# Optimization experiments

Hardware: AMD Instinct MI355X
Metric: run time of the kernel (lower is better)

## Reference

```python
import jax, jax.numpy as jnp
import numpy as np

B, H, W, C = 8, 32, 32, 512


def setup_inputs() -> dict:
    key = jax.random.key(0)
    ks = jax.random.split(key, 7)
    x = jax.random.normal(ks[0], (B, H, W, C), dtype=jnp.float32)
    conv_w = jax.random.normal(ks[1], (C, C), dtype=jnp.float32) * 0.02
    conv_b = jnp.zeros((C,), dtype=jnp.float32)
    q_w = jax.random.normal(ks[2], (C, C), dtype=jnp.float32) * 0.02
    q_b = jnp.zeros((C,), dtype=jnp.float32)
    k_w = jax.random.normal(ks[3], (C, C), dtype=jnp.float32) * 0.02
    k_b = jnp.zeros((C,), dtype=jnp.float32)
    return {"x": x, "conv_w": conv_w, "conv_b": conv_b,
            "q_w": q_w, "q_b": q_b, "k_w": k_w, "k_b": k_b}


def reference(x, conv_w, conv_b, q_w, q_b, k_w, k_b):
    # x: [B,H,W,C] channels-last (torch permutes to BCHW; we keep BHWC).
    b, h, w, c = x.shape
    hw = h * w
    scale = 1.0 / (c ** 0.5)
    # 1x1 conv + residual (weight layout: [out_ch, in_ch])
    xr = jnp.einsum('bhwc,oc->bhwo', x, conv_w) + conv_b + x
    # query / key 1x1 convs, flattened to (B*HW, C)
    q = (jnp.einsum('bhwc,oc->bhwo', xr, q_w) + q_b).reshape(b * hw, c)
    k = (jnp.einsum('bhwc,oc->bhwo', xr, k_w) + k_b).reshape(b * hw, c)
    # cross-batch affinity: (B*HW, B*HW)
    aff = (q @ k.T) * scale
    # per-(query-batch, pixel) block sums over key batches: (B, HW, B)
    s = aff.reshape(b, hw, b, hw).sum(-1)
    total = s.sum(-1)                                   # sum over all keys
    own = s[jnp.arange(b), :, jnp.arange(b)]            # own-batch block sum, (B, HW)
    rep = (total - own) / ((b - 1) * hw)                # masked mean excluding own block
    rmin = rep.min(axis=1, keepdims=True)
    rmax = rep.max(axis=1, keepdims=True)
    rep = (rep - rmin) / (rmax - rmin)                  # per-batch min-max norm
    thresh = 0.65
    return jax.nn.sigmoid((rep - thresh) / 0.15)        # (B, HW)
```

## Files before the change

### kernel.cpp

```cpp
#include <hip/hip_runtime.h>
#include <math.h>


#define BATCH 8
#define HW    1024
#define CH    512
#define SPLITS 64

__device__ __forceinline__ float dot4(float4 a, float4 b) {
    return a.x * b.x + a.y * b.y + a.z * b.z + a.w * b.w;
}

__global__ void k_xsum(const float* __restrict__ x, float* __restrict__ part) {
    int b = blockIdx.x >> 5, s = blockIdx.x & 31;
    int rg = threadIdx.x >> 7, col = threadIdx.x & 127;
    const float4* x4 = (const float4*)(x + ((size_t)(b * HW + s * 32 + rg * 8)) * CH);
    float4 acc; acc.x = acc.y = acc.z = acc.w = 0.f;
    #pragma unroll
    for (int r = 0; r < 8; ++r) {
        float4 v = x4[r * 128 + col];
        acc.x += v.x; acc.y += v.y; acc.z += v.z; acc.w += v.w;
    }
    __shared__ float4 sh[384];
    if (rg > 0) sh[(rg - 1) * 128 + col] = acc;
    __syncthreads();
    if (rg == 0) {
        #pragma unroll
        for (int j = 0; j < 3; ++j) {
            float4 o = sh[j * 128 + col];
            acc.x += o.x; acc.y += o.y; acc.z += o.z; acc.w += o.w;
        }
        ((float4*)part)[(size_t)(b * 32 + s) * 128 + col] = acc;
    }
}

__global__ void k_red(const float* __restrict__ part, float* __restrict__ xsum) {
    int b = blockIdx.x >> 2, chunk = blockIdx.x & 3;
    int c4 = threadIdx.x & 31, sg = threadIdx.x >> 5;
    const float4* p4 = (const float4*)part;
    float4 acc; acc.x = acc.y = acc.z = acc.w = 0.f;
    #pragma unroll
    for (int j = 0; j < 4; ++j) {
        int s = sg * 4 + j;
        float4 v = p4[(size_t)(b * 32 + s) * 128 + chunk * 32 + c4];
        acc.x += v.x; acc.y += v.y; acc.z += v.z; acc.w += v.w;
    }
    __shared__ float4 sh[8][32];
    sh[sg][c4] = acc;
    __syncthreads();
    if (threadIdx.x < 32) {
        float4 t = sh[0][c4];
        #pragma unroll
        for (int g = 1; g < 8; ++g) {
            float4 v = sh[g][c4];
            t.x += v.x; t.y += v.y; t.z += v.z; t.w += v.w;
        }
        ((float4*)xsum)[b * 128 + chunk * 32 + c4] = t;
    }
}

__global__ void k_t1(const float* __restrict__ xsum, const float* __restrict__ conv_w,
                     const float* __restrict__ conv_b, float* __restrict__ t1g) {
    int t = threadIdx.x;
    int b = blockIdx.x >> 7;
    int wv = t >> 6, lane = t & 63;
    __shared__ float ysh[CH];
    for (int c = t; c < CH; c += 256) {
        float tot = 0.f;
        #pragma unroll
        for (int bb = 0; bb < BATCH; ++bb) tot += xsum[bb * CH + c];
        ysh[c] = tot - xsum[b * CH + c];
    }
    __syncthreads();
    const float4* y4 = (const float4*)ysh;
    float4 ya = y4[lane], yb = y4[lane + 64];
    int o = (blockIdx.x & 127) * 4 + wv;
    const float4* w4 = (const float4*)(conv_w + (size_t)o * CH);
    float acc = dot4(ya, w4[lane]) + dot4(yb, w4[lane + 64]);
    #pragma unroll
    for (int off = 32; off; off >>= 1) acc += __shfl_xor(acc, off);
    if (lane == 0) t1g[b * CH + o] = acc + ysh[o] + 7168.f * conv_b[o];
}

__global__ void k_t2(const float* __restrict__ t1g, const float* __restrict__ k_w,
                     const float* __restrict__ k_b, float* __restrict__ t2g) {
    int t = threadIdx.x;
    int b = blockIdx.x >> 7;
    int wv = t >> 6, lane = t & 63;
    __shared__ float t1sh[CH];
    for (int c = t; c < CH; c += 256) t1sh[c] = t1g[b * CH + c];
    __syncthreads();
    const float4* a4 = (const float4*)t1sh;
    float4 aa = a4[lane], ab = a4[lane + 64];
    int o = (blockIdx.x & 127) * 4 + wv;
    const float4* w4 = (const float4*)(k_w + (size_t)o * CH);
    float acc = dot4(aa, w4[lane]) + dot4(ab, w4[lane + 64]);
    #pragma unroll
    for (int off = 32; off; off >>= 1) acc += __shfl_xor(acc, off);
    if (lane == 0) t2g[b * CH + o] = acc + 7168.f * k_b[o];
}

__global__ void k_wv(const float* __restrict__ t2g, const float* __restrict__ q_w,
                     float* __restrict__ wg) {
    int b = blockIdx.x >> 3, qc = blockIdx.x & 7;
    int t = threadIdx.x;
    __shared__ float t2sh[CH];
    __shared__ float ps[512];
    t2sh[t] = t2g[b * CH + t];
    __syncthreads();
    int c = qc * 64 + (t & 63), r0 = (t >> 6) * 64;
    float acc = 0.f;
    #pragma unroll 8
    for (int j = 0; j < 64; ++j) acc += q_w[(size_t)(r0 + j) * CH + c] * t2sh[r0 + j];
    ps[t] = acc;
    __syncthreads();
    if (t < 64) {
        float s = 0.f;
        #pragma unroll
        for (int k2 = 0; k2 < 8; ++k2) s += ps[k2 * 64 + t];
        wg[b * CH + qc * 64 + t] = s;
    }
}

__global__ void k_uv(const float* __restrict__ wg, const float* __restrict__ conv_w,
                     float* __restrict__ u) {
    int b = blockIdx.x >> 3, qc = blockIdx.x & 7;
    int t = threadIdx.x;
    __shared__ float wsh[CH];
    __shared__ float ps[512];
    wsh[t] = wg[b * CH + t];
    __syncthreads();
    int c = qc * 64 + (t & 63), r0 = (t >> 6) * 64;
    float acc = 0.f;
    #pragma unroll 8
    for (int j = 0; j < 64; ++j) acc += conv_w[(size_t)(r0 + j) * CH + c] * wsh[r0 + j];
    ps[t] = acc;
    __syncthreads();
    if (t < 64) {
        float s = 0.f;
        #pragma unroll
        for (int k2 = 0; k2 < 8; ++k2) s += ps[k2 * 64 + t];
        u[b * CH + qc * 64 + t] = s + wsh[qc * 64 + t];
    }
}

__global__ void k_dpass(const float* __restrict__ x, const float* __restrict__ u,
                        float* __restrict__ dvals, float* __restrict__ bmn,
                        float* __restrict__ bmx) {
    int s = blockIdx.x, b = blockIdx.y;
    int lane = threadIdx.x & 63, wv = threadIdx.x >> 6;
    const float4* u4 = (const float4*)(u + b * CH);
    float4 ua = u4[lane], ub = u4[lane + 64];
    __shared__ float sd[16];
    #pragma unroll
    for (int it = 0; it < 4; ++it) {
        int row = s * 16 + it * 4 + wv;
        const float4* x4 = (const float4*)(x + ((size_t)(b * HW + row)) * CH);
        float acc = dot4(x4[lane], ua) + dot4(x4[lane + 64], ub);
        #pragma unroll
        for (int off = 32; off; off >>= 1) acc += __shfl_xor(acc, off);
        if (lane == 0) {
            dvals[b * HW + row] = acc;
            sd[it * 4 + wv] = acc;
        }
    }
    __syncthreads();
    if (threadIdx.x == 0) {
        float mn = sd[0], mx = sd[0];
        #pragma unroll
        for (int i = 1; i < 16; ++i) {
            mn = fminf(mn, sd[i]); mx = fmaxf(mx, sd[i]);
        }
        bmn[b * SPLITS + s] = mn;
        bmx[b * SPLITS + s] = mx;
    }
}

__global__ void k_out(const float* __restrict__ dvals, const float* __restrict__ bmn,
                      const float* __restrict__ bmx, float* __restrict__ out) {
    int b = blockIdx.x, t = threadIdx.x;
    __shared__ float smn, smx;
    if (t < 64) {
        float mn = bmn[b * SPLITS + t];
        float mx = bmx[b * SPLITS + t];
        #pragma unroll
        for (int off = 32; off; off >>= 1) {
            mn = fminf(mn, __shfl_xor(mn, off));
            mx = fmaxf(mx, __shfl_xor(mx, off));
        }
        if (t == 0) { smn = mn; smx = mx; }
    }
    __syncthreads();
    float rmin = smn, inv = 1.f / (smx - smn);
    for (int i = t; i < HW; i += blockDim.x) {
        float d = dvals[b * HW + i];
        float rn = (d - rmin) * inv;
        float z = (rn - 0.65f) * (1.f / 0.15f);
        out[b * HW + i] = 1.f / (1.f + expf(-z));
    }
}

extern "C" void kernel_launch(void* const* d_in, const int* in_sizes, int n_in,
                              void* d_out, int out_size, void* d_ws, size_t ws_size,
                              hipStream_t stream) {
    const float* x      = (const float*)d_in[0];
    const float* conv_w = (const float*)d_in[1];
    const float* conv_b = (const float*)d_in[2];
    const float* q_w    = (const float*)d_in[3];
    const float* k_w    = (const float*)d_in[5];
    const float* k_b    = (const float*)d_in[6];
    float* out = (float*)d_out;

    float* ws    = (float*)d_ws;
    float* part  = ws;
    float* xsum  = part + 256 * CH;
    float* t1g   = xsum + BATCH * CH;
    float* t2g   = t1g + BATCH * CH;
    float* wg    = t2g + BATCH * CH;
    float* u     = wg  + BATCH * CH;
    float* dvals = u   + BATCH * CH;
    float* bmn   = dvals + BATCH * HW;
    float* bmx   = bmn + BATCH * SPLITS;

    hipLaunchKernelGGL(k_xsum,  dim3(256),           dim3(512), 0, stream, x, part);
    hipLaunchKernelGGL(k_red,   dim3(32),            dim3(256), 0, stream, part, xsum);
    hipLaunchKernelGGL(k_t1,    dim3(1024),          dim3(256), 0, stream, xsum, conv_w, conv_b, t1g);
    hipLaunchKernelGGL(k_t2,    dim3(1024),          dim3(256), 0, stream, t1g, k_w, k_b, t2g);
    hipLaunchKernelGGL(k_wv,    dim3(64),            dim3(512), 0, stream, t2g, q_w, wg);
    hipLaunchKernelGGL(k_uv,    dim3(64),            dim3(512), 0, stream, wg, conv_w, u);
    hipLaunchKernelGGL(k_dpass, dim3(SPLITS, BATCH), dim3(256), 0, stream, x, u, dvals, bmn, bmx);
    hipLaunchKernelGGL(k_out,   dim3(BATCH),         dim3(256), 0, stream, dvals, bmn, bmx, out);
}
```

Before: 98.59 us.

## Fuse two-stage column sum into one kernel and widen small kernels

The partial-sum kernel and its separate reduction kernel become one kernel: each block owns a 32-column chunk of one batch, sums all 1024 rows in registers, and reduces through shared memory. This removes a launch and the round trip through the partials workspace. It also vectorises the shared-memory staging in k_t1 and k_t2 with float4 and spreads k_out over 64 blocks instead of 8. The risk is that the fused column sum runs only 128 blocks with strided 128-byte row segments, which may lower achieved memory bandwidth on the 16 MB read.

```diff
diff --git a/kernel.cpp b/kernel.cpp
--- a/kernel.cpp
+++ b/kernel.cpp
@@ -11,51 +11,39 @@
     return a.x * b.x + a.y * b.y + a.z * b.z + a.w * b.w;
 }
 
-__global__ void k_xsum(const float* __restrict__ x, float* __restrict__ part) {
-    int b = blockIdx.x >> 5, s = blockIdx.x & 31;
-    int rg = threadIdx.x >> 7, col = threadIdx.x & 127;
-    const float4* x4 = (const float4*)(x + ((size_t)(b * HW + s * 32 + rg * 8)) * CH);
+__global__ void k_xsum(const float* __restrict__ x, float* __restrict__ xsum) {
+    int b = blockIdx.x >> 4, chunk = blockIdx.x & 15;
+    int t = threadIdx.x;
+    int col4 = t & 7, rg = t >> 3;
+    const float4* x4 = (const float4*)(x + (size_t)b * HW * CH) + chunk * 8 + col4;
     float4 acc; acc.x = acc.y = acc.z = acc.w = 0.f;
     #pragma unroll
-    for (int r = 0; r < 8; ++r) {
-        float4 v = x4[r * 128 + col];
+    for (int i = 0; i < 16; ++i) {
+        float4 v = x4[(size_t)(rg + (i << 6)) * 128];
         acc.x += v.x; acc.y += v.y; acc.z += v.z; acc.w += v.w;
     }
-    __shared__ float4 sh[384];
-    if (rg > 0) sh[(rg - 1) * 128 + col] = acc;
-    __syncthreads();
-    if (rg == 0) {
-        #pragma unroll
-        for (int j = 0; j < 3; ++j) {
-            float4 o = sh[j * 128 + col];
-            acc.x += o.x; acc.y += o.y; acc.z += o.z; acc.w += o.w;
-        }
-        ((float4*)part)[(size_t)(b * 32 + s) * 128 + col] = acc;
-    }
-}
-
-__global__ void k_red(const float* __restrict__ part, float* __restrict__ xsum) {
-    int b = blockIdx.x >> 2, chunk = blockIdx.x & 3;
-    int c4 = threadIdx.x & 31, sg = threadIdx.x >> 5;
-    const float4* p4 = (const float4*)part;
-    float4 acc; acc.x = acc.y = acc.z = acc.w = 0.f;
-    #pragma unroll
-    for (int j = 0; j < 4; ++j) {
-        int s = sg * 4 + j;
-        float4 v = p4[(size_t)(b * 32 + s) * 128 + chunk * 32 + c4];
-        acc.x += v.x; acc.y += v.y; acc.z += v.z; acc.w += v.w;
-    }
-    __shared__ float4 sh[8][32];
-    sh[sg][c4] = acc;
-    __syncthreads();
-    if (threadIdx.x < 32) {
-        float4 t = sh[0][c4];
-        #pragma unroll
-        for (int g = 1; g < 8; ++g) {
-            float4 v = sh[g][c4];
-            t.x += v.x; t.y += v.y; t.z += v.z; t.w += v.w;
-        }
-        ((float4*)xsum)[b * 128 + chunk * 32 + c4] = t;
+    __shared__ float4 sh[64][8];
+    sh[rg][col4] = acc;
+    __syncthreads();
+    if (t < 64) {
+        int c4 = t & 7, seg = t >> 3;
+        float4 a = sh[seg * 8][c4];
+        #pragma unroll
+        for (int j = 1; j < 8; ++j) {
+            float4 v = sh[seg * 8 + j][c4];
+            a.x += v.x; a.y += v.y; a.z += v.z; a.w += v.w;
+        }
+        sh[seg][c4] = a;
+    }
+    __syncthreads();
+    if (t < 8) {
+        float4 a = sh[0][t];
+        #pragma unroll
+        for (int j = 1; j < 8; ++j) {
+            float4 v = sh[j][t];
+            a.x += v.x; a.y += v.y; a.z += v.z; a.w += v.w;
+        }
+        ((float4*)xsum)[b * 128 + chunk * 8 + t] = a;
     }
 }
 
@@ -64,22 +52,29 @@
     int t = threadIdx.x;
     int b = blockIdx.x >> 7;
     int wv = t >> 6, lane = t & 63;
-    __shared__ float ysh[CH];
-    for (int c = t; c < CH; c += 256) {
-        float tot = 0.f;
-        #pragma unroll
-        for (int bb = 0; bb < BATCH; ++bb) tot += xsum[bb * CH + c];
-        ysh[c] = tot - xsum[b * CH + c];
-    }
-    __syncthreads();
-    const float4* y4 = (const float4*)ysh;
-    float4 ya = y4[lane], yb = y4[lane + 64];
+    __shared__ float4 ysh[128];
+    if (t < 128) {
+        const float4* xs4 = (const float4*)xsum;
+        float4 tot; tot.x = tot.y = tot.z = tot.w = 0.f;
+        float4 own; own.x = own.y = own.z = own.w = 0.f;
+        #pragma unroll
+        for (int bb = 0; bb < BATCH; ++bb) {
+            float4 v = xs4[bb * 128 + t];
+            tot.x += v.x; tot.y += v.y; tot.z += v.z; tot.w += v.w;
+            if (bb == b) own = v;
+        }
+        float4 y; y.x = tot.x - own.x; y.y = tot.y - own.y;
+        y.z = tot.z - own.z; y.w = tot.w - own.w;
+        ysh[t] = y;
+    }
+    __syncthreads();
+    float4 ya = ysh[lane], yb = ysh[lane + 64];
     int o = (blockIdx.x & 127) * 4 + wv;
     const float4* w4 = (const float4*)(conv_w + (size_t)o * CH);
     float acc = dot4(ya, w4[lane]) + dot4(yb, w4[lane + 64]);
     #pragma unroll
     for (int off = 32; off; off >>= 1) acc += __shfl_xor(acc, off);
-    if (lane == 0) t1g[b * CH + o] = acc + ysh[o] + 7168.f * conv_b[o];
+    if (lane == 0) t1g[b * CH + o] = acc + ((const float*)ysh)[o] + 7168.f * conv_b[o];
 }
 
 __global__ void k_t2(const float* __restrict__ t1g, const float* __restrict__ k_w,
@@ -87,11 +82,10 @@
     int t = threadIdx.x;
     int b = blockIdx.x >> 7;
     int wv = t >> 6, lane = t & 63;
-    __shared__ float t1sh[CH];
-    for (int c = t; c < CH; c += 256) t1sh[c] = t1g[b * CH + c];
-    __syncthreads();
-    const float4* a4 = (const float4*)t1sh;
-    float4 aa = a4[lane], ab = a4[lane + 64];
+    __shared__ float4 ash[128];
+    if (t < 128) ash[t] = ((const float4*)(t1g + b * CH))[t];
+    __syncthreads();
+    float4 aa = ash[lane], ab = ash[lane + 64];
     int o = (blockIdx.x & 127) * 4 + wv;
     const float4* w4 = (const float4*)(k_w + (size_t)o * CH);
     float acc = dot4(aa, w4[lane]) + dot4(ab, w4[lane + 64]);
@@ -178,7 +172,8 @@
 
 __global__ void k_out(const float* __restrict__ dvals, const float* __restrict__ bmn,
                       const float* __restrict__ bmx, float* __restrict__ out) {
-    int b = blockIdx.x, t = threadIdx.x;
+    int b = blockIdx.x >> 3, chunk = blockIdx.x & 7;
+    int t = threadIdx.x;
     __shared__ float smn, smx;
     if (t < 64) {
         float mn = bmn[b * SPLITS + t];
@@ -192,12 +187,11 @@
     }
     __syncthreads();
     float rmin = smn, inv = 1.f / (smx - smn);
-    for (int i = t; i < HW; i += blockDim.x) {
-        float d = dvals[b * HW + i];
-        float rn = (d - rmin) * inv;
-        float z = (rn - 0.65f) * (1.f / 0.15f);
-        out[b * HW + i] = 1.f / (1.f + expf(-z));
-    }
+    int i = chunk * 128 + t;
+    float d = dvals[b * HW + i];
+    float rn = (d - rmin) * inv;
+    float z = (rn - 0.65f) * (1.f / 0.15f);
+    out[b * HW + i] = 1.f / (1.f + expf(-z));
 }
 
 extern "C" void kernel_launch(void* const* d_in, const int* in_sizes, int n_in,
@@ -212,8 +206,7 @@
     float* out = (float*)d_out;
 
     float* ws    = (float*)d_ws;
-    float* part  = ws;
-    float* xsum  = part + 256 * CH;
+    float* xsum  = ws;
     float* t1g   = xsum + BATCH * CH;
     float* t2g   = t1g + BATCH * CH;
     float* wg    = t2g + BATCH * CH;
@@ -222,12 +215,11 @@
     float* bmn   = dvals + BATCH * HW;
     float* bmx   = bmn + BATCH * SPLITS;
 
-    hipLaunchKernelGGL(k_xsum,  dim3(256),           dim3(512), 0, stream, x, part);
-    hipLaunchKernelGGL(k_red,   dim3(32),            dim3(256), 0, stream, part, xsum);
+    hipLaunchKernelGGL(k_xsum,  dim3(128),           dim3(512), 0, stream, x, xsum);
     hipLaunchKernelGGL(k_t1,    dim3(1024),          dim3(256), 0, stream, xsum, conv_w, conv_b, t1g);
     hipLaunchKernelGGL(k_t2,    dim3(1024),          dim3(256), 0, stream, t1g, k_w, k_b, t2g);
     hipLaunchKernelGGL(k_wv,    dim3(64),            dim3(512), 0, stream, t2g, q_w, wg);
     hipLaunchKernelGGL(k_uv,    dim3(64),            dim3(512), 0, stream, wg, conv_w, u);
     hipLaunchKernelGGL(k_dpass, dim3(SPLITS, BATCH), dim3(256), 0, stream, x, u, dvals, bmn, bmx);
-    hipLaunchKernelGGL(k_out,   dim3(BATCH),         dim3(256), 0, stream, dvals, bmn, bmx, out);
-}
+    hipLaunchKernelGGL(k_out,   dim3(64),            dim3(128), 0, stream, dvals, bmn, bmx, out);
+}
```

Result: no change. 97.38 us (-1.2%).
